# Kernel tuning notes

Hardware: AMD Instinct MI355X
Metric: run time of the kernel (lower is better)

## Reference

```python
import jax, jax.numpy as jnp
import numpy as np

N_NODES = 100000
N_EDGES = 3200000
N_GRAPHS = 512
F_IN = 128
HID = 256
N_LABELS = 10


def setup_inputs() -> dict:
    key = jax.random.key(0)
    ks = jax.random.split(key, 16)
    x = jax.random.normal(ks[0], (N_NODES, F_IN), dtype=jnp.float32)
    edge_index = jax.random.randint(ks[1], (2, N_EDGES), 0, N_NODES)
    batch = jnp.sort(jax.random.randint(ks[2], (N_NODES,), 0, N_GRAPHS))
    dims = [(F_IN, HID), (HID, HID), (HID, HID), (HID, HID // 2), (HID // 2, HID // 2), (HID // 2, HID // 4)]
    inp = {"x": x, "edge_index": edge_index, "batch": batch, "primary_idxs_in_batch": 0}
    for i, (di, do) in enumerate(dims, 1):
        inp[f"W{i}"] = jax.random.normal(ks[2 + i], (di, do), dtype=jnp.float32) * (1.0 / np.sqrt(di))
        inp[f"b{i}"] = jnp.zeros((do,), dtype=jnp.float32)
    inp["Wlin"] = jax.random.normal(ks[12], (HID // 4, N_LABELS), dtype=jnp.float32) * (1.0 / np.sqrt(HID // 4))
    inp["blin"] = jnp.zeros((N_LABELS,), dtype=jnp.float32)
    return inp


def _gcn_conv(h, W, b, src, dst, norm):
    # dense transform first (smaller of the two sides), then normalized scatter-aggregate
    m = (h @ W)[src] * norm[:, None]  # [E+N, C_out]
    return jax.ops.segment_sum(m, dst, num_segments=N_NODES) + b


def reference(x, edge_index, batch, primary_idxs_in_batch,
              W1, b1, W2, b2, W3, b3, W4, b4, W5, b5, W6, b6, Wlin, blin):
    loops = jnp.arange(N_NODES, dtype=edge_index.dtype)
    src = jnp.concatenate([edge_index[0], loops])  # A + I (self loops)
    dst = jnp.concatenate([edge_index[1], loops])
    deg = jax.ops.segment_sum(jnp.ones_like(dst, dtype=x.dtype), dst, num_segments=N_NODES)
    dinv = jnp.where(deg > 0, jax.lax.rsqrt(deg), 0.0)
    norm = dinv[src] * dinv[dst]  # D^-1/2 (A+I) D^-1/2 edge weights

    h = jax.nn.relu(_gcn_conv(x, W1, b1, src, dst, norm))
    h = jax.nn.relu(_gcn_conv(h, W2, b2, src, dst, norm))
    h = jax.nn.relu(_gcn_conv(h, W3, b3, src, dst, norm))
    h = jax.nn.relu(_gcn_conv(h, W4, b4, src, dst, norm))
    h = jax.nn.relu(_gcn_conv(h, W5, b5, src, dst, norm))
    h = _gcn_conv(h, W6, b6, src, dst, norm)

    # primary_idxs_in_batch is falsy (0) -> global_mean_pool path
    s = jax.ops.segment_sum(h, batch, num_segments=N_GRAPHS)
    cnt = jax.ops.segment_sum(jnp.ones((N_NODES,), dtype=h.dtype), batch, num_segments=N_GRAPHS)
    pooled = s / jnp.maximum(cnt, 1.0)[:, None]  # [G, HID//4]

    logits = pooled @ Wlin + blin  # [G, labels]
    return (jax.nn.log_softmax(logits, axis=1), jax.nn.softmax(logits, axis=1))
```

## Files before the change

### kernel.cpp

```cpp
#include <hip/hip_runtime.h>
#include <math.h>

#define NN 100000
#define NE 3200000
#define NG 512
#define NBK 782
#define EBLK 782

typedef __attribute__((ext_vector_type(8))) short short8;
typedef __attribute__((ext_vector_type(4))) float f32x4;
typedef __attribute__((ext_vector_type(2))) float f32x2;

__device__ __forceinline__ float bf2f(unsigned short h){
  return __uint_as_float(((unsigned int)h) << 16);
}
__device__ __forceinline__ unsigned short f2bf(float f){
  unsigned int u = __float_as_uint(f);
  unsigned int r = (u + 0x7fffu + ((u >> 16) & 1u)) >> 16;
  return (unsigned short)r;
}
__device__ __forceinline__ void unpack16(uint4 v, float* f){
  f32x2 p;
  p = __builtin_amdgcn_cvt_pk_f32_fp8(v.x, 0); f[0]=p[0];  f[1]=p[1];
  p = __builtin_amdgcn_cvt_pk_f32_fp8(v.x, 1); f[2]=p[0];  f[3]=p[1];
  p = __builtin_amdgcn_cvt_pk_f32_fp8(v.y, 0); f[4]=p[0];  f[5]=p[1];
  p = __builtin_amdgcn_cvt_pk_f32_fp8(v.y, 1); f[6]=p[0];  f[7]=p[1];
  p = __builtin_amdgcn_cvt_pk_f32_fp8(v.z, 0); f[8]=p[0];  f[9]=p[1];
  p = __builtin_amdgcn_cvt_pk_f32_fp8(v.z, 1); f[10]=p[0]; f[11]=p[1];
  p = __builtin_amdgcn_cvt_pk_f32_fp8(v.w, 0); f[12]=p[0]; f[13]=p[1];
  p = __builtin_amdgcn_cvt_pk_f32_fp8(v.w, 1); f[14]=p[0]; f[15]=p[1];
}
__device__ __forceinline__ unsigned char f2fp8(float v){
  int p = __builtin_amdgcn_cvt_pk_fp8_f32(v, v, 0, 0);
  return (unsigned char)p;
}

__global__ __launch_bounds__(256) void hist2_k(const int* __restrict__ ei,
    int* __restrict__ cnt, int* __restrict__ btot){
  __shared__ int lh[NBK];
  int t = threadIdx.x, b = blockIdx.x;
  for (int i=t; i<NBK; i+=256) lh[i] = 0;
  __syncthreads();
  int base = b*4096;
  #pragma unroll
  for (int u=0; u<16; u++){
    int e = base + u*256 + t;
    if (e < NE) atomicAdd(&lh[ei[NE + e] >> 7], 1);
  }
  __syncthreads();
  for (int i=t; i<NBK; i+=256){
    int v = lh[i];
    cnt[b*NBK + i] = v;
    if (v) atomicAdd(&btot[i], v);
  }
}
__global__ void bscan2_k(const int* __restrict__ btot, int* __restrict__ bptr){
  __shared__ int sc[1024];
  int t = threadIdx.x;
  int v = (t < NBK) ? btot[t] : 0;
  sc[t] = v; __syncthreads();
  for (int off=1; off<1024; off<<=1){
    int u = (t>=off) ? sc[t-off] : 0;
    __syncthreads(); sc[t] += u; __syncthreads();
  }
  if (t < NBK) bptr[t] = sc[t] - v;
  if (t == 1023) bptr[NBK] = sc[1023];
}
__global__ __launch_bounds__(256) void bkpfx_k(int* __restrict__ cnt, const int* __restrict__ bptr){
  __shared__ int sc[256];
  int b = blockIdx.x, t = threadIdx.x;
  int carry = bptr[b];
  for (int base=0; base<EBLK; base+=256){
    int blk = base + t;
    int v = (blk < EBLK) ? cnt[blk*NBK + b] : 0;
    sc[t] = v; __syncthreads();
    for (int off=1; off<256; off<<=1){
      int u = (t>=off) ? sc[t-off] : 0;
      __syncthreads(); sc[t] += u; __syncthreads();
    }
    if (blk < EBLK) cnt[blk*NBK + b] = carry + sc[t] - v;
    carry += sc[255];
    __syncthreads();
  }
}
__global__ __launch_bounds__(256) void scat2_k(const int* __restrict__ ei,
    const int* __restrict__ cnt, unsigned int* __restrict__ ebuf){
  __shared__ int lh[NBK];
  __shared__ int lo[NBK];
  int t = threadIdx.x, b = blockIdx.x;
  for (int i=t; i<NBK; i+=256){ lh[i] = 0; lo[i] = cnt[b*NBK + i]; }
  __syncthreads();
  int base = b*4096;
  #pragma unroll
  for (int u=0; u<16; u++){
    int e = base + u*256 + t;
    if (e < NE){
      int s = ei[e], d = ei[NE + e];
      int bk = d >> 7;
      int r = atomicAdd(&lh[bk], 1);
      ebuf[lo[bk] + r] = (unsigned)s | ((unsigned)(d & 127) << 17);
    }
  }
}
__global__ __launch_bounds__(256) void bcsr_k(const unsigned int* __restrict__ ebuf,
    const int* __restrict__ bptr, int* __restrict__ rp, float* __restrict__ dinv,
    int* __restrict__ col){
  __shared__ int cnt[128];
  __shared__ int off[128];
  __shared__ int sc[128];
  int b = blockIdx.x, t = threadIdx.x;
  int nbase = b << 7;
  int beg = bptr[b], end = bptr[b+1];
  if (t < 128) cnt[t] = 0;
  __syncthreads();
  for (int e = beg + t; e < end; e += 256)
    atomicAdd(&cnt[ebuf[e] >> 17], 1);
  __syncthreads();
  int v = (t < 128) ? cnt[t] : 0;
  if (t < 128) sc[t] = v;
  __syncthreads();
  for (int o2=1; o2<128; o2<<=1){
    int u = (t < 128 && t >= o2) ? sc[t-o2] : 0;
    __syncthreads();
    if (t < 128) sc[t] += u;
    __syncthreads();
  }
  if (t < 128){
    int node = nbase + t;
    if (node < NN){
      int ex = beg + sc[t] - v;
      rp[node] = ex;
      off[t] = ex;
      dinv[node] = rsqrtf((float)(v + 1));
      cnt[t] = 0;
    }
  }
  if (b == ((NN-1) >> 7) && t == 0) rp[NN] = end;
  __syncthreads();
  for (int e = beg + t; e < end; e += 256){
    unsigned int sd = ebuf[e];
    int li = sd >> 17;
    int pos = off[li] + atomicAdd(&cnt[li], 1);
    col[pos] = (int)(sd & 0x1FFFF);
  }
}

__global__ void f2q_k(const float* __restrict__ in, unsigned char* __restrict__ out, int n4){
  int i = blockIdx.x*256 + threadIdx.x;
  if (i < n4){
    float4 v = ((const float4*)in)[i];
    int p = __builtin_amdgcn_cvt_pk_fp8_f32(v.x, v.y, 0, 0);
    p = __builtin_amdgcn_cvt_pk_fp8_f32(v.z, v.w, p, 1);
    ((unsigned int*)out)[i] = (unsigned int)p;
  }
}
__global__ void wswz_all_k(const float* W1, const float* W2, const float* W3,
                           const float* W4, const float* W5, const float* W6,
                           unsigned short* O1, unsigned short* O2, unsigned short* O3,
                           unsigned short* O4, unsigned short* O5, unsigned short* O6){
  int cfg = blockIdx.y;
  int K, N; const float* W; unsigned short* out;
  switch(cfg){
    case 0: K=128; N=256; W=W1; out=O1; break;
    case 1: K=256; N=256; W=W2; out=O2; break;
    case 2: K=256; N=256; W=W3; out=O3; break;
    case 3: K=256; N=128; W=W4; out=O4; break;
    case 4: K=128; N=128; W=W5; out=O5; break;
    default:K=128; N=64;  W=W6; out=O6; break;
  }
  int idx = blockIdx.x*256 + threadIdx.x;
  int total = K*N/8;
  if (idx >= total) return;
  int l = idx & 15;
  int t = idx >> 4; int q = t & 3; t >>= 2;
  int NT = N/16;
  int nt = t % NT, kt = t / NT;
  int kbase = kt*32 + q*8, n = nt*16 + l;
  short8 o;
  #pragma unroll
  for (int j=0;j<8;j++) o[j] = (short)f2bf(W[(size_t)(kbase+j)*N + n]);
  *(short8*)(out + (size_t)idx*8) = o;
}

template<int C, bool SRC_SCALE, bool RELU, bool HAS_BIAS>
__global__ __launch_bounds__(256) void spmm8_k(const unsigned char* __restrict__ in,
    unsigned short* __restrict__ out,
    const int* __restrict__ rp, const int* __restrict__ col,
    const float* __restrict__ dinv, const float* __restrict__ bias)
{
  constexpr int LPR = C/16;
  constexpr int RPW = 64/LPR;
  constexpr int RPB = 4*RPW;
  int tid = threadIdx.x;
  int wv = tid >> 6, lane = tid & 63;
  int sub = lane / LPR, li = lane % LPR;
  int row = blockIdx.x*RPB + wv*RPW + sub;
  if (row >= NN) return;
  int beg = rp[row], end = rp[row+1];
  float di = dinv[row];
  int co = li*16;
  const unsigned char* inb = in + co;
  float acc[16], tmp[16];
  unpack16(*(const uint4*)(inb + (size_t)row*C), acc);
  if (SRC_SCALE){
    #pragma unroll
    for (int v=0;v<16;v++) acc[v] *= di;
  }
  int j = beg;
  for (; j+8 <= end; j += 8){
    int s[8]; uint4 v[8]; float wgt[8];
    #pragma unroll
    for (int u=0;u<8;u++) s[u] = col[j+u];
    #pragma unroll
    for (int u=0;u<8;u++) v[u] = *(const uint4*)(inb + (size_t)s[u]*C);
    if (SRC_SCALE){
      #pragma unroll
      for (int u=0;u<8;u++) wgt[u] = dinv[s[u]];
    }
    #pragma unroll
    for (int u=0;u<8;u++){
      unpack16(v[u], tmp);
      float w = SRC_SCALE ? wgt[u] : 1.f;
      #pragma unroll
      for (int vv=0;vv<16;vv++) acc[vv] = fmaf(w, tmp[vv], acc[vv]);
    }
  }
  for (; j < end; j++){
    int ss = col[j];
    uint4 v = *(const uint4*)(inb + (size_t)ss*C);
    float w = SRC_SCALE ? dinv[ss] : 1.f;
    unpack16(v, tmp);
    #pragma unroll
    for (int vv=0;vv<16;vv++) acc[vv] = fmaf(w, tmp[vv], acc[vv]);
  }
  float bb[16];
  if (HAS_BIAS){
    #pragma unroll
    for (int u=0;u<4;u++) *(float4*)&bb[u*4] = *(const float4*)(bias + co + u*4);
  }
  #pragma unroll
  for (int v=0;v<16;v++){
    acc[v] *= di;
    if (HAS_BIAS) acc[v] += bb[v];
    if (RELU) acc[v] = fmaxf(acc[v], 0.f);
  }
  uint4 o0, o1;
  o0.x = (unsigned int)f2bf(acc[0])  | ((unsigned int)f2bf(acc[1])<<16);
  o0.y = (unsigned int)f2bf(acc[2])  | ((unsigned int)f2bf(acc[3])<<16);
  o0.z = (unsigned int)f2bf(acc[4])  | ((unsigned int)f2bf(acc[5])<<16);
  o0.w = (unsigned int)f2bf(acc[6])  | ((unsigned int)f2bf(acc[7])<<16);
  o1.x = (unsigned int)f2bf(acc[8])  | ((unsigned int)f2bf(acc[9])<<16);
  o1.y = (unsigned int)f2bf(acc[10]) | ((unsigned int)f2bf(acc[11])<<16);
  o1.z = (unsigned int)f2bf(acc[12]) | ((unsigned int)f2bf(acc[13])<<16);
  o1.w = (unsigned int)f2bf(acc[14]) | ((unsigned int)f2bf(acc[15])<<16);
  unsigned short* op = out + (size_t)row*C + co;
  *(uint4*)op = o0;
  *(uint4*)(op + 8) = o1;
}

template<int K, int N, int EPI>
__global__ __launch_bounds__(256) void mgemm_k(const unsigned short* __restrict__ A,
    const unsigned short* __restrict__ Bsw,
    const float* __restrict__ aux, unsigned short* __restrict__ Cb,
    unsigned char* __restrict__ Cq, int M)
{
  constexpr int NT = 4;
  constexpr int KT = K/32;
  constexpr int NTF = N/16;
  __shared__ short8 Bl[KT*NT*64];
  int tid = threadIdx.x;
  int w = tid >> 6, lane = tid & 63;
  int l = lane & 15, q = lane >> 4;
  int nb0 = blockIdx.x * 64;
  int rb = blockIdx.y*256 + w*64;
  {
    const short8* bsrc = (const short8*)Bsw;
    for (int i = tid; i < KT*NT*64; i += 256){
      int kt = i >> 8;
      int rem = i & 255;
      Bl[i] = bsrc[(kt*NTF + (nb0 >> 4))*64 + rem];
    }
  }
  const unsigned short* ap[4];
  #pragma unroll
  for (int rt=0; rt<4; rt++){
    int r = min(rb + rt*16 + l, M-1);
    ap[rt] = A + (size_t)r*K + q*8;
  }
  f32x4 acc[4][NT];
  #pragma unroll
  for (int rt=0; rt<4; rt++)
    #pragma unroll
    for (int nt=0; nt<NT; nt++) acc[rt][nt] = (f32x4){0,0,0,0};
  short8 a[4], an[4];
  #pragma unroll
  for (int rt=0; rt<4; rt++) a[rt] = *(const short8*)(ap[rt]);
  __syncthreads();
  for (int kt=0; kt<KT; kt++){
    if (kt+1 < KT){
      #pragma unroll
      for (int rt=0; rt<4; rt++) an[rt] = *(const short8*)(ap[rt] + (kt+1)*32);
    }
    const short8* bl = &Bl[kt << 8];
    #pragma unroll
    for (int nt=0; nt<NT; nt++){
      short8 bf = bl[nt*64 + q*16 + l];
      acc[0][nt] = __builtin_amdgcn_mfma_f32_16x16x32_bf16(a[0], bf, acc[0][nt], 0,0,0);
      acc[1][nt] = __builtin_amdgcn_mfma_f32_16x16x32_bf16(a[1], bf, acc[1][nt], 0,0,0);
      acc[2][nt] = __builtin_amdgcn_mfma_f32_16x16x32_bf16(a[2], bf, acc[2][nt], 0,0,0);
      acc[3][nt] = __builtin_amdgcn_mfma_f32_16x16x32_bf16(a[3], bf, acc[3][nt], 0,0,0);
    }
    #pragma unroll
    for (int rt=0; rt<4; rt++) a[rt] = an[rt];
  }
  #pragma unroll
  for (int rt=0; rt<4; rt++){
    int rbb = rb + rt*16;
    #pragma unroll
    for (int nt=0; nt<NT; nt++){
      f32x4 av = acc[rt][nt];
      int n = nb0 + nt*16 + l;
      #pragma unroll
      for (int r=0;r<4;r++){
        int row = rbb + q*4 + r;
        if (row < M){
          float v = av[r];
          if (EPI == 0){
            v = fmaxf(v + aux[n], 0.f);
            Cb[(size_t)row*N + n] = f2bf(v);
          } else {
            v *= aux[row];
            Cq[(size_t)row*N + n] = f2fp8(v);
          }
        }
      }
    }
  }
}

__global__ __launch_bounds__(256) void poolhead_k(const unsigned short* __restrict__ h,
    const int* __restrict__ batch, const float* __restrict__ Wlin,
    const float* __restrict__ blin, float* __restrict__ out)
{
  __shared__ int range[2];
  __shared__ float red[4][64];
  __shared__ float pl[64];
  int g = blockIdx.x;
  if (threadIdx.x < 2){
    int target = g + threadIdx.x;
    int lo = 0, hi = NN;
    while (lo < hi){ int m = (lo+hi) >> 1; if (batch[m] < target) lo = m+1; else hi = m; }
    range[threadIdx.x] = lo;
  }
  __syncthreads();
  int lo = range[0], hi = range[1];
  int ch = threadIdx.x & 63, rg = threadIdx.x >> 6;
  float s = 0.f;
  for (int r = lo + rg; r < hi; r += 4) s += bf2f(h[(size_t)r*64 + ch]);
  red[rg][ch] = s; __syncthreads();
  if (rg == 0){
    float tot = red[0][ch] + red[1][ch] + red[2][ch] + red[3][ch];
    pl[ch] = tot / fmaxf((float)(hi - lo), 1.f);
  }
  __syncthreads();
  if (threadIdx.x == 0){
    float l[10];
    #pragma unroll
    for (int j=0;j<10;j++) l[j] = blin[j];
    for (int c=0;c<64;c++){
      float p = pl[c];
      #pragma unroll
      for (int j=0;j<10;j++) l[j] = fmaf(p, Wlin[c*10 + j], l[j]);
    }
    float mx = l[0];
    #pragma unroll
    for (int j=1;j<10;j++) mx = fmaxf(mx, l[j]);
    float e[10]; float se = 0.f;
    #pragma unroll
    for (int j=0;j<10;j++){ e[j] = expf(l[j]-mx); se += e[j]; }
    float lse = logf(se);
    #pragma unroll
    for (int j=0;j<10;j++){
      out[g*10 + j]         = l[j] - mx - lse;
      out[NG*10 + g*10 + j] = e[j] / se;
    }
  }
}

extern "C" void kernel_launch(void* const* d_in, const int* in_sizes, int n_in,
                              void* d_out, int out_size, void* d_ws, size_t ws_size,
                              hipStream_t stream)
{
  const float* x     = (const float*)d_in[0];
  const int*   ei    = (const int*)  d_in[1];
  const int*   batch = (const int*)  d_in[2];
  const float* W1=(const float*)d_in[4],  *b1=(const float*)d_in[5];
  const float* W2=(const float*)d_in[6],  *b2=(const float*)d_in[7];
  const float* W3=(const float*)d_in[8],  *b3=(const float*)d_in[9];
  const float* W4=(const float*)d_in[10], *b4=(const float*)d_in[11];
  const float* W5=(const float*)d_in[12], *b5=(const float*)d_in[13];
  const float* W6=(const float*)d_in[14], *b6=(const float*)d_in[15];
  const float* Wl=(const float*)d_in[16], *bl=(const float*)d_in[17];
  float* out = (float*)d_out;

  char* ws = (char*)d_ws;
  unsigned short* hA  = (unsigned short*)(ws + 0);
  unsigned short* hB  = (unsigned short*)(ws + 51200000);
  unsigned char*  hQ  = (unsigned char*) (ws + 102400000);
  unsigned char*  xq  = (unsigned char*) (ws + 128000000);
  int*   col   = (int*)  (ws + 140800000);
  unsigned int* ebuf = (unsigned int*)(ws + 153600000);
  int*   rp    = (int*)  (ws + 166400000);
  float* dinv  = (float*)(ws + 166800016);
  unsigned short* W1s = (unsigned short*)(ws + 167200016);
  unsigned short* W2s = (unsigned short*)(ws + 167265552);
  unsigned short* W3s = (unsigned short*)(ws + 167396624);
  unsigned short* W4s = (unsigned short*)(ws + 167527696);
  unsigned short* W5s = (unsigned short*)(ws + 167593232);
  unsigned short* W6s = (unsigned short*)(ws + 167626000);
  int*   btot  = (int*)  (ws + 167642896);
  int*   bptr  = (int*)  (ws + 167646032);
  int*   cnt   = (int*)  (ws + 167649184);

  hipMemsetAsync(btot, 0, NBK*4, stream);

  hist2_k <<<EBLK, 256, 0, stream>>>(ei, cnt, btot);
  bscan2_k<<<1, 1024, 0, stream>>>(btot, bptr);
  bkpfx_k <<<NBK, 256, 0, stream>>>(cnt, bptr);
  scat2_k <<<EBLK, 256, 0, stream>>>(ei, cnt, ebuf);
  bcsr_k  <<<NBK, 256, 0, stream>>>(ebuf, bptr, rp, dinv, col);

  wswz_all_k<<<dim3(32,6), 256, 0, stream>>>(W1,W2,W3,W4,W5,W6, W1s,W2s,W3s,W4s,W5s,W6s);
  f2q_k<<<(NN*128/4 + 255)/256, 256, 0, stream>>>(x, xq, NN*128/4);

  const int SQ256 = (NN + 15)/16, SQ128 = (NN + 31)/32, SQ64 = (NN + 63)/64;
  const int GX = (NN + 255)/256;

  spmm8_k<128,true,false,false><<<SQ128,256,0,stream>>>(xq, hA, rp, col, dinv, nullptr);
  mgemm_k<128,256,0><<<dim3(4,GX),256,0,stream>>>(hA, W1s, b1, hB, nullptr, NN);
  mgemm_k<256,256,1><<<dim3(4,GX),256,0,stream>>>(hB, W2s, dinv, nullptr, hQ, NN);
  spmm8_k<256,false,true,true><<<SQ256,256,0,stream>>>(hQ, hA, rp, col, dinv, b2);
  mgemm_k<256,256,1><<<dim3(4,GX),256,0,stream>>>(hA, W3s, dinv, nullptr, hQ, NN);
  spmm8_k<256,false,true,true><<<SQ256,256,0,stream>>>(hQ, hB, rp, col, dinv, b3);
  mgemm_k<256,128,1><<<dim3(2,GX),256,0,stream>>>(hB, W4s, dinv, nullptr, hQ, NN);
  spmm8_k<128,false,true,true><<<SQ128,256,0,stream>>>(hQ, hA, rp, col, dinv, b4);
  mgemm_k<128,128,1><<<dim3(2,GX),256,0,stream>>>(hA, W5s, dinv, nullptr, hQ, NN);
  spmm8_k<128,false,true,true><<<SQ128,256,0,stream>>>(hQ, hB, rp, col, dinv, b5);
  mgemm_k<128,64,1><<<dim3(1,GX),256,0,stream>>>(hB, W6s, dinv, nullptr, hQ, NN);
  spmm8_k<64,false,false,true><<<SQ64,256,0,stream>>>(hQ, hA, rp, col, dinv, b6);

  poolhead_k<<<NG, 256, 0, stream>>>(hA, batch, Wl, bl, out);
}
```

Measured before the change: 1.086 ms.

## Sort rows by degree per bucket and split wide SpMM columns across grid

bcsr_k now computes, for each 128-node bucket, a permutation that orders nodes by in-degree, and stores it in the reused cnt buffer. The SpMM kernels read their row through this permutation, so rows with similar neighbor counts share a wavefront. This is meant to cut divergence and tail imbalance inside each wavefront. The 256-wide aggregations are also split into two 128-column halves along blockIdx.y, which doubles the number of blocks but gathers each neighbor row twice, once per half, and may lower L2 reuse.

```diff
diff --git a/kernel.cpp b/kernel.cpp
--- a/kernel.cpp
+++ b/kernel.cpp
@@ -104,10 +104,11 @@
 }
 __global__ __launch_bounds__(256) void bcsr_k(const unsigned int* __restrict__ ebuf,
     const int* __restrict__ bptr, int* __restrict__ rp, float* __restrict__ dinv,
-    int* __restrict__ col){
+    int* __restrict__ col, int* __restrict__ permg){
   __shared__ int cnt[128];
   __shared__ int off[128];
   __shared__ int sc[128];
+  __shared__ int dg[128];
   int b = blockIdx.x, t = threadIdx.x;
   int nbase = b << 7;
   int beg = bptr[b], end = bptr[b+1];
@@ -117,7 +118,10 @@
     atomicAdd(&cnt[ebuf[e] >> 17], 1);
   __syncthreads();
   int v = (t < 128) ? cnt[t] : 0;
-  if (t < 128) sc[t] = v;
+  if (t < 128){
+    sc[t] = v;
+    dg[t] = ((nbase + t) < NN) ? v : 0x7FFFFFFF;
+  }
   __syncthreads();
   for (int o2=1; o2<128; o2<<=1){
     int u = (t < 128 && t >= o2) ? sc[t-o2] : 0;
@@ -134,6 +138,14 @@
       dinv[node] = rsqrtf((float)(v + 1));
       cnt[t] = 0;
     }
+    int d = dg[t];
+    int rk = 0;
+    #pragma unroll 4
+    for (int u=0; u<128; u++){
+      int du = dg[u];
+      rk += (int)((du < d) || (du == d && u < t));
+    }
+    permg[nbase + rk] = node;
   }
   if (b == ((NN-1) >> 7) && t == 0) rp[NN] = end;
   __syncthreads();
@@ -182,26 +194,28 @@
   *(short8*)(out + (size_t)idx*8) = o;
 }
 
-template<int C, bool SRC_SCALE, bool RELU, bool HAS_BIAS>
+template<int RS, int W, bool SRC_SCALE, bool RELU, bool HAS_BIAS>
 __global__ __launch_bounds__(256) void spmm8_k(const unsigned char* __restrict__ in,
     unsigned short* __restrict__ out,
     const int* __restrict__ rp, const int* __restrict__ col,
-    const float* __restrict__ dinv, const float* __restrict__ bias)
+    const float* __restrict__ dinv, const int* __restrict__ perm,
+    const float* __restrict__ bias)
 {
-  constexpr int LPR = C/16;
+  constexpr int LPR = W/16;
   constexpr int RPW = 64/LPR;
   constexpr int RPB = 4*RPW;
   int tid = threadIdx.x;
   int wv = tid >> 6, lane = tid & 63;
   int sub = lane / LPR, li = lane % LPR;
-  int row = blockIdx.x*RPB + wv*RPW + sub;
+  int pidx = blockIdx.x*RPB + wv*RPW + sub;
+  int row = perm[pidx];
   if (row >= NN) return;
   int beg = rp[row], end = rp[row+1];
   float di = dinv[row];
-  int co = li*16;
+  int co = blockIdx.y*W + li*16;
   const unsigned char* inb = in + co;
   float acc[16], tmp[16];
-  unpack16(*(const uint4*)(inb + (size_t)row*C), acc);
+  unpack16(*(const uint4*)(inb + (size_t)row*RS), acc);
   if (SRC_SCALE){
     #pragma unroll
     for (int v=0;v<16;v++) acc[v] *= di;
@@ -212,7 +226,7 @@
     #pragma unroll
     for (int u=0;u<8;u++) s[u] = col[j+u];
     #pragma unroll
-    for (int u=0;u<8;u++) v[u] = *(const uint4*)(inb + (size_t)s[u]*C);
+    for (int u=0;u<8;u++) v[u] = *(const uint4*)(inb + (size_t)s[u]*RS);
     if (SRC_SCALE){
       #pragma unroll
       for (int u=0;u<8;u++) wgt[u] = dinv[s[u]];
@@ -227,7 +241,7 @@
   }
   for (; j < end; j++){
     int ss = col[j];
-    uint4 v = *(const uint4*)(inb + (size_t)ss*C);
+    uint4 v = *(const uint4*)(inb + (size_t)ss*RS);
     float w = SRC_SCALE ? dinv[ss] : 1.f;
     unpack16(v, tmp);
     #pragma unroll
@@ -253,7 +267,7 @@
   o1.y = (unsigned int)f2bf(acc[10]) | ((unsigned int)f2bf(acc[11])<<16);
   o1.z = (unsigned int)f2bf(acc[12]) | ((unsigned int)f2bf(acc[13])<<16);
   o1.w = (unsigned int)f2bf(acc[14]) | ((unsigned int)f2bf(acc[15])<<16);
-  unsigned short* op = out + (size_t)row*C + co;
+  unsigned short* op = out + (size_t)row*RS + co;
   *(uint4*)op = o0;
   *(uint4*)(op + 8) = o1;
 }
@@ -421,6 +435,7 @@
   int*   btot  = (int*)  (ws + 167642896);
   int*   bptr  = (int*)  (ws + 167646032);
   int*   cnt   = (int*)  (ws + 167649184);
+  int*   perm  = cnt;
 
   hipMemsetAsync(btot, 0, NBK*4, stream);
 
@@ -428,26 +443,27 @@
   bscan2_k<<<1, 1024, 0, stream>>>(btot, bptr);
   bkpfx_k <<<NBK, 256, 0, stream>>>(cnt, bptr);
   scat2_k <<<EBLK, 256, 0, stream>>>(ei, cnt, ebuf);
-  bcsr_k  <<<NBK, 256, 0, stream>>>(ebuf, bptr, rp, dinv, col);
+  bcsr_k  <<<NBK, 256, 0, stream>>>(ebuf, bptr, rp, dinv, col, perm);
 
   wswz_all_k<<<dim3(32,6), 256, 0, stream>>>(W1,W2,W3,W4,W5,W6, W1s,W2s,W3s,W4s,W5s,W6s);
   f2q_k<<<(NN*128/4 + 255)/256, 256, 0, stream>>>(x, xq, NN*128/4);
 
-  const int SQ256 = (NN + 15)/16, SQ128 = (NN + 31)/32, SQ64 = (NN + 63)/64;
+  const int GW128 = (NN + 31)/32;
+  const int GW64  = (NN + 63)/64;
   const int GX = (NN + 255)/256;
 
-  spmm8_k<128,true,false,false><<<SQ128,256,0,stream>>>(xq, hA, rp, col, dinv, nullptr);
+  spmm8_k<128,128,true,false,false><<<dim3(GW128,1),256,0,stream>>>(xq, hA, rp, col, dinv, perm, nullptr);
   mgemm_k<128,256,0><<<dim3(4,GX),256,0,stream>>>(hA, W1s, b1, hB, nullptr, NN);
   mgemm_k<256,256,1><<<dim3(4,GX),256,0,stream>>>(hB, W2s, dinv, nullptr, hQ, NN);
-  spmm8_k<256,false,true,true><<<SQ256,256,0,stream>>>(hQ, hA, rp, col, dinv, b2);
+  spmm8_k<256,128,false,true,true><<<dim3(GW128,2),256,0,stream>>>(hQ, hA, rp, col, dinv, perm, b2);
   mgemm_k<256,256,1><<<dim3(4,GX),256,0,stream>>>(hA, W3s, dinv, nullptr, hQ, NN);
-  spmm8_k<256,false,true,true><<<SQ256,256,0,stream>>>(hQ, hB, rp, col, dinv, b3);
+  spmm8_k<256,128,false,true,true><<<dim3(GW128,2),256,0,stream>>>(hQ, hB, rp, col, dinv, perm, b3);
   mgemm_k<256,128,1><<<dim3(2,GX),256,0,stream>>>(hB, W4s, dinv, nullptr, hQ, NN);
-  spmm8_k<128,false,true,true><<<SQ128,256,0,stream>>>(hQ, hA, rp, col, dinv, b4);
+  spmm8_k<128,128,false,true,true><<<dim3(GW128,1),256,0,stream>>>(hQ, hA, rp, col, dinv, perm, b4);
   mgemm_k<128,128,1><<<dim3(2,GX),256,0,stream>>>(hA, W5s, dinv, nullptr, hQ, NN);
-  spmm8_k<128,false,true,true><<<SQ128,256,0,stream>>>(hQ, hB, rp, col, dinv, b5);
+  spmm8_k<128,128,false,true,true><<<dim3(GW128,1),256,0,stream>>>(hQ, hB, rp, col, dinv, perm, b5);
   mgemm_k<128,64,1><<<dim3(1,GX),256,0,stream>>>(hB, W6s, dinv, nullptr, hQ, NN);
-  spmm8_k<64,false,false,true><<<SQ64,256,0,stream>>>(hQ, hA, rp, col, dinv, b6);
+  spmm8_k<64,64,false,false,true><<<dim3(GW64,1),256,0,stream>>>(hQ, hA, rp, col, dinv, perm, b6);
 
   poolhead_k<<<NG, 256, 0, stream>>>(hA, batch, Wl, bl, out);
 }
```

Result: no change. 1.079 ms (-0.6%).
